# Kernel tuning notes

Hardware: AMD Instinct MI355X
Metric: run time of the kernel (lower is better)

## Reference

```python
import jax, jax.numpy as jnp
import numpy as np

NX = 1024
N_HEAD = 16
HEAD_DIM = NX // N_HEAD
MASKED_BIAS = -10000.0


def setup_inputs() -> dict:
    key = jax.random.key(0)
    k1, k2, k3 = jax.random.split(key, 3)
    hidden_states = jax.random.normal(k1, (2, 2048, NX), dtype=jnp.float32)
    # Conv1D weights: stored [in, out], y = x @ W + b (like torch addmm)
    c_attn_w = jax.random.normal(k2, (NX, 3 * NX), dtype=jnp.float32) * 0.02
    c_attn_b = jnp.zeros((3 * NX,), dtype=jnp.float32)
    c_proj_w = jax.random.normal(k3, (NX, NX), dtype=jnp.float32) * 0.02
    c_proj_b = jnp.zeros((NX,), dtype=jnp.float32)
    return {
        "hidden_states": hidden_states,
        "c_attn_w": c_attn_w,
        "c_attn_b": c_attn_b,
        "c_proj_w": c_proj_w,
        "c_proj_b": c_proj_b,
    }


def reference(hidden_states, c_attn_w, c_attn_b, c_proj_w, c_proj_b):
    B, S, _ = hidden_states.shape
    qkv = hidden_states @ c_attn_w + c_attn_b  # [B, S, 3*NX]
    q, k, v = jnp.split(qkv, 3, axis=-1)
    # split heads -> [B, H, S, D]
    def split_heads(x):
        return x.reshape(B, S, N_HEAD, HEAD_DIM).transpose(0, 2, 1, 3)
    q, k, v = split_heads(q), split_heads(k), split_heads(v)
    # scores scaled by sqrt(head_dim) (v.size(-1)**0.5 in original)
    w = jnp.einsum("bhqd,bhkd->bhqk", q, k) / jnp.sqrt(jnp.float32(HEAD_DIM))
    # causal mask (nd == ns here since no past)
    causal = jnp.tril(jnp.ones((S, S), dtype=bool))
    w = jnp.where(causal[None, None, :, :], w, jnp.float32(MASKED_BIAS))
    w = jax.nn.softmax(w, axis=-1)
    a = jnp.einsum("bhqk,bhkd->bhqd", w, v)  # [B, H, S, D]
    # merge heads
    a = a.transpose(0, 2, 1, 3).reshape(B, S, NX)
    out = a @ c_proj_w + c_proj_b
    return out
```

## Files before the change

kernel.cpp:

```cpp
#include <hip/hip_runtime.h>
#include <hip/hip_bf16.h>
#include <cmath>

typedef __attribute__((ext_vector_type(8))) short bf16x8;
typedef __attribute__((ext_vector_type(4))) float f32x4;

#define NXC 1024
#define NH 16
#define HD 64
#define BATCH 2
#define SEQ 2048
#define TOK (BATCH * SEQ)

__device__ __forceinline__ ushort f2bf(float f) {
  unsigned u;
  asm("v_cvt_pk_bf16_f32 %0, %1, %2" : "=v"(u) : "v"(f), "v"(f));
  return (ushort)u;
}

__device__ __forceinline__ void gload_lds16(const void* g, void* lds) {
  __builtin_amdgcn_global_load_lds(
      (const __attribute__((address_space(1))) void*)g,
      (__attribute__((address_space(3))) void*)lds, 16, 0, 0);
}

__device__ __forceinline__ float fast_exp2(float x) {
  float r;
  asm("v_exp_f32 %0, %1" : "=v"(r) : "v"(x));
  return r;
}

template <int CTRL>
__device__ __forceinline__ float dpp_mov(float x) {
  return __builtin_bit_cast(
      float, __builtin_amdgcn_mov_dpp(__builtin_bit_cast(int, x), CTRL, 0xF, 0xF, true));
}
__device__ __forceinline__ float red16_max(float x) {
  x = fmaxf(x, dpp_mov<0x121>(x));
  x = fmaxf(x, dpp_mov<0x122>(x));
  x = fmaxf(x, dpp_mov<0x124>(x));
  x = fmaxf(x, dpp_mov<0x128>(x));
  return x;
}
__device__ __forceinline__ float red16_sum(float x) {
  x += dpp_mov<0x121>(x);
  x += dpp_mov<0x122>(x);
  x += dpp_mov<0x124>(x);
  x += dpp_mov<0x128>(x);
  return x;
}

__global__ __launch_bounds__(256) void k_convert(const float* __restrict__ in,
                                                 ushort* __restrict__ out) {
  int i = (blockIdx.x * 256 + threadIdx.x) * 4;
  float4 v = *(const float4*)(in + i);
  ushort4 o;
  o.x = f2bf(v.x); o.y = f2bf(v.y); o.z = f2bf(v.z); o.w = f2bf(v.w);
  int row = i >> 10;
  int dst = (i & ~63) | ((i & 63) ^ ((row & 7) << 3));
  *(ushort4*)(out + dst) = o;
}

__global__ __launch_bounds__(256) void k_transpose_w(const float* __restrict__ in,
                                                     ushort* __restrict__ out,
                                                     int Kd, int Nd) {
  __shared__ float t[32][33];
  int n0 = blockIdx.x * 32, k0 = blockIdx.y * 32;
  int tx = threadIdx.x & 31, ty = threadIdx.x >> 5;
#pragma unroll
  for (int r = 0; r < 4; ++r)
    t[tx][ty + r * 8] = in[(size_t)(k0 + ty + r * 8) * Nd + n0 + tx];
  __syncthreads();
  int nl = threadIdx.x >> 3, kq = (threadIdx.x & 7) * 4;
  ushort4 o;
  o.x = f2bf(t[nl][kq + 0]);
  o.y = f2bf(t[nl][kq + 1]);
  o.z = f2bf(t[nl][kq + 2]);
  o.w = f2bf(t[nl][kq + 3]);
  int row = n0 + nl, kk = k0 + kq;
  size_t dst = (size_t)row * Kd + (kk & ~63) + ((kk & 63) ^ ((row & 7) << 3));
  *(ushort4*)&out[dst] = o;
}

__global__ __launch_bounds__(256) void k_transpose_v(const ushort* __restrict__ in,
                                                     ushort* __restrict__ out) {
  __shared__ ushort t[32][33];
  int bh = blockIdx.z;
  int s0 = blockIdx.x * 32, d0 = blockIdx.y * 32;
  const ushort* ip = in + (size_t)bh * SEQ * HD;
  ushort* op = out + (size_t)bh * HD * SEQ;
  int tx = threadIdx.x & 31, ty = threadIdx.x >> 5;
#pragma unroll
  for (int r = 0; r < 4; ++r)
    t[tx][ty + r * 8] = ip[(size_t)(s0 + ty + r * 8) * HD + d0 + tx];
  __syncthreads();
  int dl = threadIdx.x >> 3, sq = (threadIdx.x & 7) * 4;
  ushort4 o;
  o.x = t[dl][sq + 0]; o.y = t[dl][sq + 1];
  o.z = t[dl][sq + 2]; o.w = t[dl][sq + 3];
  int key = (s0 + sq) ^ ((dl & 7) << 3);
  *(ushort4*)&op[(size_t)(d0 + dl) * SEQ + key] = o;
}

__global__ __launch_bounds__(256) void k_gemm_qkv(const ushort* __restrict__ A,
                                                  const ushort* __restrict__ Bt,
                                                  const float* __restrict__ bias,
                                                  ushort* __restrict__ q_ws,
                                                  ushort* __restrict__ k_ws,
                                                  ushort* __restrict__ v_tmp) {
  __shared__ ushort As[2][128 * 64];
  __shared__ ushort Bs[2][128 * 64];
  const int tid = threadIdx.x;
  const int wave = tid >> 6, lane = tid & 63;
  const int xcd = blockIdx.x & 7, loc = blockIdx.x >> 3;
  const int m0 = ((xcd >> 1) * 8 + (loc & 7)) * 128;
  const int n0 = ((xcd & 1) * 12 + (loc >> 3)) * 128;
  const int wr = (wave >> 1) * 64, wc = (wave & 1) * 64;
  const int l15 = lane & 15, lg = lane >> 4;
  const int swz = (l15 & 7) << 3;
  f32x4 acc[4][4] = {};

  auto stage = [&](int k0, int buf) {
#pragma unroll
    for (int c = 0; c < 4; ++c) {
      int offB = wave * 4096 + c * 1024 + lane * 16;
      int row = offB >> 7, colB = offB & 127;
      gload_lds16((const char*)A + (size_t)(m0 + row) * 2048 + k0 * 2 + colB,
                  (char*)As[buf] + wave * 4096 + c * 1024);
      gload_lds16((const char*)Bt + (size_t)(n0 + row) * 2048 + k0 * 2 + colB,
                  (char*)Bs[buf] + wave * 4096 + c * 1024);
    }
  };

  stage(0, 0);
  asm volatile("s_waitcnt vmcnt(0)" ::: "memory");
  __syncthreads();

  for (int kt = 0; kt < 16; ++kt) {
    const int cur = kt & 1;
    if (kt < 15) stage((kt + 1) * 64, cur ^ 1);
#pragma unroll
    for (int kc = 0; kc < 2; ++kc) {
      bf16x8 af[4], bfr[4];
#pragma unroll
      for (int i = 0; i < 4; ++i)
        af[i] = *(const bf16x8*)&As[cur][(wr + i * 16 + l15) * 64 + ((kc * 32 + lg * 8) ^ swz)];
#pragma unroll
      for (int j = 0; j < 4; ++j)
        bfr[j] = *(const bf16x8*)&Bs[cur][(wc + j * 16 + l15) * 64 + ((kc * 32 + lg * 8) ^ swz)];
#pragma unroll
      for (int i = 0; i < 4; ++i)
#pragma unroll
        for (int j = 0; j < 4; ++j)
          acc[i][j] = __builtin_amdgcn_mfma_f32_16x16x32_bf16(af[i], bfr[j], acc[i][j], 0, 0, 0);
    }
    asm volatile("s_waitcnt vmcnt(0)" ::: "memory");
    __syncthreads();
  }
#pragma unroll
  for (int j = 0; j < 4; ++j) {
    int col = n0 + wc + j * 16 + l15;
    float bv = bias[col];
    int sec = col >> 10;
    int within = col & 1023;
    int head = within >> 6, d = within & 63;
#pragma unroll
    for (int i = 0; i < 4; ++i) {
#pragma unroll
      for (int r = 0; r < 4; ++r) {
        int row = m0 + wr + i * 16 + lg * 4 + r;
        int b = row >> 11, s = row & 2047;
        float val = acc[i][j][r] + bv;
        size_t hb = ((size_t)(b * NH + head) * SEQ + s) * HD;
        if (sec == 0)      q_ws[hb + d] = f2bf(val * 0.1803368801f);
        else if (sec == 1) k_ws[hb + (d ^ ((s & 7) << 3))] = f2bf(val);
        else               v_tmp[hb + d] = f2bf(val);
      }
    }
  }
}

__global__ __launch_bounds__(256) void k_attn(const ushort* __restrict__ q_ws,
                                              const ushort* __restrict__ k_ws,
                                              const ushort* __restrict__ v_ws,
                                              ushort* __restrict__ a_ws) {
  __shared__ ushort Ks[2][64 * 64];
  __shared__ ushort Vs[2][64 * 64];
  __shared__ ushort Ps[4][2][16 * 64];
  const int p = blockIdx.x, bh = blockIdx.y;
  const int qtA = 31 - p, qtB = p;
  const int tid = threadIdx.x, wave = tid >> 6, lane = tid & 63;
  const int l15 = lane & 15, lg = lane >> 4;
  const int swz = (l15 & 7) << 3;
  const ushort* qp = q_ws + (size_t)bh * SEQ * HD;
  const ushort* kp = k_ws + (size_t)bh * SEQ * HD;
  const ushort* vp = v_ws + (size_t)bh * HD * SEQ;

  bf16x8 qfA[2], qfB[2];
  {
    int qrA = qtA * 64 + wave * 16 + l15;
    int qrB = qtB * 64 + wave * 16 + l15;
    qfA[0] = *(const bf16x8*)&qp[(size_t)qrA * HD + lg * 8];
    qfA[1] = *(const bf16x8*)&qp[(size_t)qrA * HD + 32 + lg * 8];
    qfB[0] = *(const bf16x8*)&qp[(size_t)qrB * HD + lg * 8];
    qfB[1] = *(const bf16x8*)&qp[(size_t)qrB * HD + 32 + lg * 8];
  }
  f32x4 oA[4] = {}, oB[4] = {};
  float mA[4] = {-INFINITY, -INFINITY, -INFINITY, -INFINITY};
  float mB[4] = {-INFINITY, -INFINITY, -INFINITY, -INFINITY};
  float lA[4] = {0.f, 0.f, 0.f, 0.f}, lB[4] = {0.f, 0.f, 0.f, 0.f};

  auto stage = [&](int kt, int buf) {
#pragma unroll
    for (int c = 0; c < 2; ++c) {
      int offB = wave * 2048 + c * 1024 + lane * 16;
      gload_lds16((const char*)kp + (size_t)kt * 8192 + offB,
                  (char*)Ks[buf] + offB);
      int d = offB >> 7, keyB = offB & 127;
      gload_lds16((const char*)vp + (size_t)d * (SEQ * 2) + (size_t)kt * 128 + keyB,
                  (char*)Vs[buf] + offB);
    }
  };

  auto tile_step = [&](const bf16x8* qf, f32x4* o, float* m_r, float* l_r,
                       ushort* Pw, const ushort* Kc, const ushort* Vc, bool diag) {
    f32x4 sc[4] = {};
#pragma unroll
    for (int kc = 0; kc < 2; ++kc)
#pragma unroll
      for (int f = 0; f < 4; ++f) {
        if (diag && f > wave) continue;
        bf16x8 kf = *(const bf16x8*)&Kc[(f * 16 + l15) * 64 + ((kc * 32 + lg * 8) ^ swz)];
        sc[f] = __builtin_amdgcn_mfma_f32_16x16x32_bf16(qf[kc], kf, sc[f], 0, 0, 0);
      }
    if (diag) {
#pragma unroll
      for (int f = 0; f < 4; ++f) {
        int key_rel = f * 16 + l15;
#pragma unroll
        for (int r = 0; r < 4; ++r) {
          int q_rel = wave * 16 + lg * 4 + r;
          if (key_rel > q_rel) sc[f][r] = -1e30f;
        }
      }
    }
    float pm[4];
#pragma unroll
    for (int r = 0; r < 4; ++r)
      pm[r] = fmaxf(fmaxf(sc[0][r], sc[1][r]), fmaxf(sc[2][r], sc[3][r]));
    bool need = false;
#pragma unroll
    for (int r = 0; r < 4; ++r) need |= (pm[r] > m_r[r] + 8.f);
    if (__any(need)) {
#pragma unroll
      for (int r = 0; r < 4; ++r) {
        float full = red16_max(pm[r]);
        float mn = fmaxf(m_r[r], full);
        float al = fast_exp2(m_r[r] - mn);
        m_r[r] = mn;
        l_r[r] *= al;
#pragma unroll
        for (int df = 0; df < 4; ++df) o[df][r] *= al;
      }
    }
#pragma unroll
    for (int f = 0; f < 4; ++f)
#pragma unroll
      for (int r = 0; r < 4; ++r) {
        float pv = fast_exp2(sc[f][r] - m_r[r]);
        l_r[r] += pv;
        int q = lg * 4 + r;
        Pw[q * 64 + ((f * 16 + l15) ^ ((q & 7) << 3))] = f2bf(pv);
      }
#pragma unroll
    for (int kc = 0; kc < 2; ++kc) {
      bf16x8 pf = *(const bf16x8*)&Pw[l15 * 64 + ((kc * 32 + lg * 8) ^ swz)];
#pragma unroll
      for (int df = 0; df < 4; ++df) {
        bf16x8 vf = *(const bf16x8*)&Vc[(df * 16 + l15) * 64 + ((kc * 32 + lg * 8) ^ swz)];
        o[df] = __builtin_amdgcn_mfma_f32_16x16x32_bf16(pf, vf, o[df], 0, 0, 0);
      }
    }
  };

  stage(0, 0);
  asm volatile("s_waitcnt vmcnt(0)" ::: "memory");
  __syncthreads();

  for (int kt = 0; kt <= qtA; ++kt) {
    const int cur = kt & 1;
    if (kt < qtA) stage(kt + 1, cur ^ 1);
    tile_step(qfA, oA, mA, lA, Ps[wave][0], Ks[cur], Vs[cur], kt == qtA);
    if (kt <= qtB)
      tile_step(qfB, oB, mB, lB, Ps[wave][1], Ks[cur], Vs[cur], kt == qtB);
    asm volatile("s_waitcnt vmcnt(0)" ::: "memory");
    __syncthreads();
  }

  int b = bh >> 4, head = bh & 15;
  auto epilogue = [&](f32x4* o, float* l_r, int qt) {
#pragma unroll
    for (int r = 0; r < 4; ++r) {
      float inv = 1.0f / red16_sum(l_r[r]);
      int s = qt * 64 + wave * 16 + lg * 4 + r;
#pragma unroll
      for (int df = 0; df < 4; ++df) {
        int col = head * 64 + ((df * 16 + l15) ^ ((s & 7) << 3));
        a_ws[((size_t)(b * SEQ + s)) * NXC + col] = f2bf(o[df][r] * inv);
      }
    }
  };
  epilogue(oA, lA, qtA);
  epilogue(oB, lB, qtB);
}

__global__ __launch_bounds__(256) void k_gemm_proj(const ushort* __restrict__ A,
                                                   const ushort* __restrict__ Bt,
                                                   const float* __restrict__ bias,
                                                   float* __restrict__ out) {
  __shared__ ushort As[2][128 * 64];
  __shared__ ushort Bs[2][128 * 64];
  const int tid = threadIdx.x;
  const int wave = tid >> 6, lane = tid & 63;
  const int xcd = blockIdx.x & 7, loc = blockIdx.x >> 3;
  const int m0 = ((xcd >> 1) * 8 + (loc & 7)) * 128;
  const int n0 = ((xcd & 1) * 4 + (loc >> 3)) * 128;
  const int wr = (wave >> 1) * 64, wc = (wave & 1) * 64;
  const int l15 = lane & 15, lg = lane >> 4;
  const int swz = (l15 & 7) << 3;
  f32x4 acc[4][4] = {};

  auto stage = [&](int k0, int buf) {
#pragma unroll
    for (int c = 0; c < 4; ++c) {
      int offB = wave * 4096 + c * 1024 + lane * 16;
      int row = offB >> 7, colB = offB & 127;
      gload_lds16((const char*)A + (size_t)(m0 + row) * 2048 + k0 * 2 + colB,
                  (char*)As[buf] + wave * 4096 + c * 1024);
      gload_lds16((const char*)Bt + (size_t)(n0 + row) * 2048 + k0 * 2 + colB,
                  (char*)Bs[buf] + wave * 4096 + c * 1024);
    }
  };

  stage(0, 0);
  asm volatile("s_waitcnt vmcnt(0)" ::: "memory");
  __syncthreads();

  for (int kt = 0; kt < 16; ++kt) {
    const int cur = kt & 1;
    if (kt < 15) stage((kt + 1) * 64, cur ^ 1);
#pragma unroll
    for (int kc = 0; kc < 2; ++kc) {
      bf16x8 af[4], bfr[4];
#pragma unroll
      for (int i = 0; i < 4; ++i)
        af[i] = *(const bf16x8*)&As[cur][(wr + i * 16 + l15) * 64 + ((kc * 32 + lg * 8) ^ swz)];
#pragma unroll
      for (int j = 0; j < 4; ++j)
        bfr[j] = *(const bf16x8*)&Bs[cur][(wc + j * 16 + l15) * 64 + ((kc * 32 + lg * 8) ^ swz)];
#pragma unroll
      for (int i = 0; i < 4; ++i)
#pragma unroll
        for (int j = 0; j < 4; ++j)
          acc[i][j] = __builtin_amdgcn_mfma_f32_16x16x32_bf16(af[i], bfr[j], acc[i][j], 0, 0, 0);
    }
    asm volatile("s_waitcnt vmcnt(0)" ::: "memory");
    __syncthreads();
  }
#pragma unroll
  for (int j = 0; j < 4; ++j) {
    int col = n0 + wc + j * 16 + l15;
    float bv = bias[col];
#pragma unroll
    for (int i = 0; i < 4; ++i) {
#pragma unroll
      for (int r = 0; r < 4; ++r) {
        int row = m0 + wr + i * 16 + lg * 4 + r;
        out[(size_t)row * NXC + col] = acc[i][j][r] + bv;
      }
    }
  }
}

extern "C" void kernel_launch(void* const* d_in, const int* in_sizes, int n_in,
                              void* d_out, int out_size, void* d_ws, size_t ws_size,
                              hipStream_t stream) {
  const float* hs       = (const float*)d_in[0];
  const float* c_attn_w = (const float*)d_in[1];
  const float* c_attn_b = (const float*)d_in[2];
  const float* c_proj_w = (const float*)d_in[3];
  const float* c_proj_b = (const float*)d_in[4];
  char* ws = (char*)d_ws;
  const size_t MB = 1 << 20;
  ushort* Xb      = (ushort*)(ws + 0 * MB);
  ushort* Wt_attn = (ushort*)(ws + 8 * MB);
  ushort* Wt_proj = (ushort*)(ws + 14 * MB);
  ushort* q_ws    = (ushort*)(ws + 16 * MB);
  ushort* k_ws    = (ushort*)(ws + 24 * MB);
  ushort* v_ws    = (ushort*)(ws + 32 * MB);
  ushort* a_ws    = (ushort*)(ws + 40 * MB);
  ushort* v_tmp   = a_ws;

  k_convert<<<4096, 256, 0, stream>>>(hs, Xb);
  k_transpose_w<<<dim3(96, 32), 256, 0, stream>>>(c_attn_w, Wt_attn, 1024, 3072);
  k_transpose_w<<<dim3(32, 32), 256, 0, stream>>>(c_proj_w, Wt_proj, 1024, 1024);
  k_gemm_qkv<<<768, 256, 0, stream>>>(Xb, Wt_attn, c_attn_b, q_ws, k_ws, v_tmp);
  k_transpose_v<<<dim3(64, 2, 32), 256, 0, stream>>>(v_tmp, v_ws);
  k_attn<<<dim3(16, 32), 256, 0, stream>>>(q_ws, k_ws, v_ws, a_ws);
  k_gemm_proj<<<256, 256, 0, stream>>>(a_ws, Wt_proj, c_proj_b, (float*)d_out);
}
```

Measured before the change: 139.5 us.

## Fuse fp32-to-bf16 conversion of hidden states into QKV GEMM A-tile loading

Removes the separate k_convert kernel and its intermediate bf16 buffer. The QKV GEMM now loads fp32 hidden-state rows into registers, converts them to bf16 in-kernel and writes them swizzled into a single-buffered LDS A tile, prefetching two k-steps ahead. B tiles stay double-buffered via direct global-to-LDS loads. This saves one launch plus a write and re-read of the converted activations. In exchange the GEMM reads fp32 data (twice the bytes per A tile, re-read by each of the 24 column blocks), uses more registers, and needs an extra barrier per iteration.

```diff
diff --git a/kernel.cpp b/kernel.cpp
--- a/kernel.cpp
+++ b/kernel.cpp
@@ -48,17 +48,6 @@
   x += dpp_mov<0x124>(x);
   x += dpp_mov<0x128>(x);
   return x;
-}
-
-__global__ __launch_bounds__(256) void k_convert(const float* __restrict__ in,
-                                                 ushort* __restrict__ out) {
-  int i = (blockIdx.x * 256 + threadIdx.x) * 4;
-  float4 v = *(const float4*)(in + i);
-  ushort4 o;
-  o.x = f2bf(v.x); o.y = f2bf(v.y); o.z = f2bf(v.z); o.w = f2bf(v.w);
-  int row = i >> 10;
-  int dst = (i & ~63) | ((i & 63) ^ ((row & 7) << 3));
-  *(ushort4*)(out + dst) = o;
 }
 
 __global__ __launch_bounds__(256) void k_transpose_w(const float* __restrict__ in,
@@ -102,13 +91,13 @@
   *(ushort4*)&op[(size_t)(d0 + dl) * SEQ + key] = o;
 }
 
-__global__ __launch_bounds__(256) void k_gemm_qkv(const ushort* __restrict__ A,
-                                                  const ushort* __restrict__ Bt,
-                                                  const float* __restrict__ bias,
-                                                  ushort* __restrict__ q_ws,
-                                                  ushort* __restrict__ k_ws,
-                                                  ushort* __restrict__ v_tmp) {
-  __shared__ ushort As[2][128 * 64];
+__global__ __launch_bounds__(256, 3) void k_gemm_qkv(const float* __restrict__ X,
+                                                     const ushort* __restrict__ Bt,
+                                                     const float* __restrict__ bias,
+                                                     ushort* __restrict__ q_ws,
+                                                     ushort* __restrict__ k_ws,
+                                                     ushort* __restrict__ v_tmp) {
+  __shared__ ushort As[128 * 64];
   __shared__ ushort Bs[2][128 * 64];
   const int tid = threadIdx.x;
   const int wave = tid >> 6, lane = tid & 63;
@@ -118,33 +107,53 @@
   const int wr = (wave >> 1) * 64, wc = (wave & 1) * 64;
   const int l15 = lane & 15, lg = lane >> 4;
   const int swz = (l15 & 7) << 3;
+  const int arow = wave * 32 + lg;
+  const int akcol = l15 * 4;
   f32x4 acc[4][4] = {};
-
-  auto stage = [&](int k0, int buf) {
+  float4 areg[8];
+
+  auto a_issue = [&](int kt) {
+#pragma unroll
+    for (int c = 0; c < 8; ++c)
+      areg[c] = *(const float4*)&X[(size_t)(m0 + arow + c * 4) * 1024 + kt * 64 + akcol];
+  };
+  auto a_write = [&]() {
+#pragma unroll
+    for (int c = 0; c < 8; ++c) {
+      int row = arow + c * 4;
+      unsigned p0, p1;
+      asm("v_cvt_pk_bf16_f32 %0, %1, %2" : "=v"(p0) : "v"(areg[c].x), "v"(areg[c].y));
+      asm("v_cvt_pk_bf16_f32 %0, %1, %2" : "=v"(p1) : "v"(areg[c].z), "v"(areg[c].w));
+      *(uint2*)&As[row * 64 + (akcol ^ ((row & 7) << 3))] = make_uint2(p0, p1);
+    }
+  };
+  auto stageB = [&](int kt, int buf) {
 #pragma unroll
     for (int c = 0; c < 4; ++c) {
       int offB = wave * 4096 + c * 1024 + lane * 16;
       int row = offB >> 7, colB = offB & 127;
-      gload_lds16((const char*)A + (size_t)(m0 + row) * 2048 + k0 * 2 + colB,
-                  (char*)As[buf] + wave * 4096 + c * 1024);
-      gload_lds16((const char*)Bt + (size_t)(n0 + row) * 2048 + k0 * 2 + colB,
+      gload_lds16((const char*)Bt + (size_t)(n0 + row) * 2048 + kt * 128 + colB,
                   (char*)Bs[buf] + wave * 4096 + c * 1024);
     }
   };
 
-  stage(0, 0);
-  asm volatile("s_waitcnt vmcnt(0)" ::: "memory");
-  __syncthreads();
-
+  a_issue(0);
+  stageB(0, 0);
+  a_write();
+  a_issue(1);
+  asm volatile("s_waitcnt vmcnt(8) lgkmcnt(0)" ::: "memory");
+  __builtin_amdgcn_s_barrier();
+
+#pragma unroll 1
   for (int kt = 0; kt < 16; ++kt) {
     const int cur = kt & 1;
-    if (kt < 15) stage((kt + 1) * 64, cur ^ 1);
+    if (kt < 15) stageB(kt + 1, cur ^ 1);
 #pragma unroll
     for (int kc = 0; kc < 2; ++kc) {
       bf16x8 af[4], bfr[4];
 #pragma unroll
       for (int i = 0; i < 4; ++i)
-        af[i] = *(const bf16x8*)&As[cur][(wr + i * 16 + l15) * 64 + ((kc * 32 + lg * 8) ^ swz)];
+        af[i] = *(const bf16x8*)&As[(wr + i * 16 + l15) * 64 + ((kc * 32 + lg * 8) ^ swz)];
 #pragma unroll
       for (int j = 0; j < 4; ++j)
         bfr[j] = *(const bf16x8*)&Bs[cur][(wc + j * 16 + l15) * 64 + ((kc * 32 + lg * 8) ^ swz)];
@@ -154,9 +163,15 @@
         for (int j = 0; j < 4; ++j)
           acc[i][j] = __builtin_amdgcn_mfma_f32_16x16x32_bf16(af[i], bfr[j], acc[i][j], 0, 0, 0);
     }
-    asm volatile("s_waitcnt vmcnt(0)" ::: "memory");
     __syncthreads();
-  }
+    if (kt < 15) {
+      a_write();
+      if (kt < 14) a_issue(kt + 2);
+      asm volatile("s_waitcnt lgkmcnt(0)" ::: "memory");
+      __builtin_amdgcn_s_barrier();
+    }
+  }
+
 #pragma unroll
   for (int j = 0; j < 4; ++j) {
     int col = n0 + wc + j * 16 + l15;
@@ -392,7 +407,6 @@
   const float* c_proj_b = (const float*)d_in[4];
   char* ws = (char*)d_ws;
   const size_t MB = 1 << 20;
-  ushort* Xb      = (ushort*)(ws + 0 * MB);
   ushort* Wt_attn = (ushort*)(ws + 8 * MB);
   ushort* Wt_proj = (ushort*)(ws + 14 * MB);
   ushort* q_ws    = (ushort*)(ws + 16 * MB);
@@ -401,10 +415,9 @@
   ushort* a_ws    = (ushort*)(ws + 40 * MB);
   ushort* v_tmp   = a_ws;
 
-  k_convert<<<4096, 256, 0, stream>>>(hs, Xb);
   k_transpose_w<<<dim3(96, 32), 256, 0, stream>>>(c_attn_w, Wt_attn, 1024, 3072);
   k_transpose_w<<<dim3(32, 32), 256, 0, stream>>>(c_proj_w, Wt_proj, 1024, 1024);
-  k_gemm_qkv<<<768, 256, 0, stream>>>(Xb, Wt_attn, c_attn_b, q_ws, k_ws, v_tmp);
+  k_gemm_qkv<<<768, 256, 0, stream>>>(hs, Wt_attn, c_attn_b, q_ws, k_ws, v_tmp);
   k_transpose_v<<<dim3(64, 2, 32), 256, 0, stream>>>(v_tmp, v_ws);
   k_attn<<<dim3(16, 32), 256, 0, stream>>>(q_ws, k_ws, v_ws, a_ws);
   k_gemm_proj<<<256, 256, 0, stream>>>(a_ws, Wt_proj, c_proj_b, (float*)d_out);
```

Result: faster. 128.7 us (-7.7%).
